# Optimization experiments

Hardware: AMD Instinct MI355X
Metric: run time of the kernel (lower is better)

The kernel has to match this reference:

```python
import jax, jax.numpy as jnp
import numpy as np

SEQ_LEN = 48
OUT_DIM = 3
EMB_DIM = 32
HID_DIM = 96
BATCH = 131072


def setup_inputs() -> dict:
    key = jax.random.key(0)
    ks = jax.random.split(key, 12)
    s_emb = 1.0 / np.sqrt(OUT_DIM)
    s_gru = 1.0 / np.sqrt(HID_DIM)
    s_out = 1.0 / np.sqrt(HID_DIM)
    u = lambda k, shp, s: jax.random.uniform(k, shp, jnp.float32, -s, s)
    return {
        "last_pos_rel": jax.random.normal(ks[0], (BATCH, OUT_DIM), jnp.float32),
        "past_encoded": jax.random.normal(ks[1], (1, BATCH, HID_DIM // 2), jnp.float32),
        "future_encoded": jax.random.normal(ks[2], (1, BATCH, HID_DIM // 2), jnp.float32),
        "W_emb": u(ks[3], (EMB_DIM, OUT_DIM), s_emb),
        "b_emb": u(ks[4], (EMB_DIM,), s_emb),
        "W_ih": u(ks[5], (3 * HID_DIM, EMB_DIM), s_gru),
        "W_hh": u(ks[6], (3 * HID_DIM, HID_DIM), s_gru),
        "b_ih": u(ks[7], (3 * HID_DIM,), s_gru),
        "b_hh": u(ks[8], (3 * HID_DIM,), s_gru),
        "W_out": u(ks[9], (OUT_DIM, HID_DIM), s_out),
        "b_out": u(ks[10], (OUT_DIM,), s_out),
    }


def reference(last_pos_rel, past_encoded, future_encoded, W_emb, b_emb,
              W_ih, W_hh, b_ih, b_hh, W_out, b_out):
    # initial hidden state: concat of the two 48-dim encodings -> (B, 96)
    h0 = jnp.concatenate([past_encoded, future_encoded], axis=2)[0]
    # initial decoder input: spatial embedding of last relative position
    x0 = last_pos_rel @ W_emb.T + b_emb  # (B, EMB)

    def step(carry, _):
        h, x = carry
        gx = x @ W_ih.T + b_ih   # (B, 3H)
        gh = h @ W_hh.T + b_hh   # (B, 3H)
        gxr, gxz, gxn = jnp.split(gx, 3, axis=-1)
        ghr, ghz, ghn = jnp.split(gh, 3, axis=-1)
        r = jax.nn.sigmoid(gxr + ghr)
        z = jax.nn.sigmoid(gxz + ghz)
        n = jnp.tanh(gxn + r * ghn)
        h_new = (1.0 - z) * n + z * h
        rel_pos = h_new @ W_out.T + b_out       # (B, 3)
        x_new = rel_pos @ W_emb.T + b_emb       # (B, EMB)
        return (h_new, x_new), rel_pos

    _, pred_traj = jax.lax.scan(step, (h0, x0), None, length=SEQ_LEN)
    return pred_traj  # (SEQ_LEN, B, 3)
```

## Files before the change

kernel.cpp:

```cpp
#include <hip/hip_runtime.h>
#include <hip/hip_bf16.h>
#include <type_traits>

#define SEQ_LEN 48
#define HID     96
#define NB      131072
#define MROWS   304
#define ABYTES  (MROWS*HID*2)
#define A_U4    (ABYTES/16)
#define COEF_OFF_F (ABYTES/4)
#define COEF_FLOATS (96*16)
#define BOUT_OFF_F (COEF_OFF_F + COEF_FLOATS)

typedef __attribute__((ext_vector_type(4))) float f32x4;
typedef __attribute__((ext_vector_type(8))) __bf16 bf16x8;
typedef unsigned int uint;
typedef unsigned short ushort;

__device__ __forceinline__ float sigm2(float xp) {
    return __builtin_amdgcn_rcpf(1.f + __builtin_amdgcn_exp2f(-xp));
}
__device__ __forceinline__ float tanh2(float yp) {
    return 1.f - 2.f * __builtin_amdgcn_rcpf(__builtin_amdgcn_exp2f(yp) + 1.f);
}
__device__ __forceinline__ uint packbf(float a, float b) {
    ushort lo = __builtin_bit_cast(ushort, __float2bfloat16(a));
    ushort hi = __builtin_bit_cast(ushort, __float2bfloat16(b));
    return (uint)lo | ((uint)hi << 16);
}

__global__ void fold_k(const float* __restrict__ W_emb, const float* __restrict__ b_emb,
                       const float* __restrict__ W_ih,  const float* __restrict__ W_hh,
                       const float* __restrict__ b_ih,  const float* __restrict__ b_hh,
                       const float* __restrict__ W_out, const float* __restrict__ b_out,
                       void* wsv)
{
    const float L2E  = 1.44269504088896340736f;
    const float L2E2 = 2.f * L2E;
    ushort* A  = (ushort*)wsv;
    float*  CF = (float*)wsv + COEF_OFF_F;
    float*  BO = (float*)wsv + BOUT_OFF_F;
    int g = blockIdx.x * 64 + threadIdx.x;
    if (g < 3) BO[g] = b_out[g];

    auto wxe_row = [&](int gg, float* w, float& bx) {
        w[0] = w[1] = w[2] = 0.f; bx = b_ih[gg];
        for (int e = 0; e < 32; e++) {
            float wi = W_ih[gg * 32 + e];
            w[0] += wi * W_emb[e * 3 + 0];
            w[1] += wi * W_emb[e * 3 + 1];
            w[2] += wi * W_emb[e * 3 + 2];
            bx   += wi * b_emb[e];
        }
    };

    if (g < MROWS) {
        float w[3] = {0.f, 0.f, 0.f}, bx = 0.f;
        if (g < 192) wxe_row(g, w, bx);
        for (int k = 0; k < HID; k++) {
            float val;
            if      (g < 192) val = (W_hh[g * HID + k] + w[0]*W_out[0*HID+k] + w[1]*W_out[1*HID+k] + w[2]*W_out[2*HID+k]) * L2E;
            else if (g < 288) val = W_hh[g * HID + k] * L2E2;
            else if (g < 291) val = W_out[(g - 288) * HID + k];
            else              val = 0.f;
            int t = g >> 4, c = k >> 5, l = (g & 15) | (((k >> 3) & 3) << 4), i = k & 7;
            A[((t * 3 + c) * 64 + l) * 8 + i] = __builtin_bit_cast(ushort, __float2bfloat16(val));
        }
    }
    if (g < 96) {
        int j = g;
        float wn[3], bxn; wxe_row(192 + j, wn, bxn);
        float wr[3], bxr; wxe_row(j,        wr, bxr);
        float wz[3], bxz; wxe_row(96 + j,   wz, bxz);
        float quads[4][4] = {
            { wn[0]*L2E2, wn[1]*L2E2, wn[2]*L2E2, bxn*L2E2 },
            { b_hh[192 + j]*L2E2,
              (bxr + b_hh[j]      + wr[0]*b_out[0] + wr[1]*b_out[1] + wr[2]*b_out[2]) * L2E,
              (bxz + b_hh[96 + j] + wz[0]*b_out[0] + wz[1]*b_out[1] + wz[2]*b_out[2]) * L2E,
              0.f },
            { wr[0]*L2E, wr[1]*L2E, wr[2]*L2E, wz[0]*L2E },
            { wz[1]*L2E, wz[2]*L2E, 0.f, 0.f }
        };
        int qj = (j >> 2) & 3;
        float* row = CF + j * 16;
        for (int L = 0; L < 4; ++L) {
            int p = (L + qj) & 3;
            row[p * 4 + 0] = quads[L][0];
            row[p * 4 + 1] = quads[L][1];
            row[p * 4 + 2] = quads[L][2];
            row[p * 4 + 3] = quads[L][3];
        }
    }
}

__global__ __launch_bounds__(256, 2)
void gru_mfma(const float* __restrict__ last_pos, const float* __restrict__ past,
              const float* __restrict__ fut, const void* __restrict__ wsv,
              float* __restrict__ out)
{
    __shared__ uint4 sb[A_U4];
    const int tid = threadIdx.x;
    const uint4* gsrc = (const uint4*)wsv;
    #pragma unroll
    for (int it = 0; it < 15; ++it) { int idx = tid + it * 256; if (idx < A_U4) sb[idx] = gsrc[idx]; }
    __syncthreads();

    const float* CF  = (const float*)wsv + COEF_OFF_F;
    const float* BOg = (const float*)wsv + BOUT_OFF_F;
    const float bo[3] = {BOg[0], BOg[1], BOg[2]};

    const int lane = tid & 63;
    const int wid  = tid >> 6;
    const int b    = lane & 15;
    const int q    = lane >> 4;
    const int rowbase = blockIdx.x * 128 + wid * 32;

    uint hpk[2][6][2];
    #pragma unroll
    for (int nt = 0; nt < 2; ++nt) {
        int row = rowbase + nt * 16 + b;
        #pragma unroll
        for (int t = 0; t < 6; ++t) {
            const float* src = (t < 3) ? (past + (size_t)row * 48 + t * 16 + q * 4)
                                       : (fut  + (size_t)row * 48 + (t - 3) * 16 + q * 4);
            f32x4 v = *(const f32x4*)src;
            hpk[nt][t][0] = packbf(v[0], v[1]);
            hpk[nt][t][1] = packbf(v[2], v[3]);
        }
    }

    const int idxA = 4 * (b | ((((q << 1) + 0) & 3) << 4));
    const int idxB = 4 * (b | ((((q << 1) + 1) & 3) << 4));
    uint4 bfu[2][3];
    auto do_exchange = [&]() {
        #pragma unroll
        for (int nt = 0; nt < 2; ++nt)
            #pragma unroll
            for (int c = 0; c < 3; ++c)
                #pragma unroll
                for (int dd = 0; dd < 4; ++dd) {
                    int idx = (dd < 2) ? idxA : idxB;
                    int va = __builtin_amdgcn_ds_bpermute(idx, (int)hpk[nt][2 * c][dd & 1]);
                    int vb = __builtin_amdgcn_ds_bpermute(idx, (int)hpk[nt][2 * c + 1][dd & 1]);
                    bfu[nt][c][dd] = (uint)((lane < 32) ? va : vb);
                }
    };
    do_exchange();

    float pc[2][3];
    #pragma unroll
    for (int nt = 0; nt < 2; ++nt) {
        int row = rowbase + nt * 16 + b;
        pc[nt][0] = last_pos[(size_t)row * 3 + 0];
        pc[nt][1] = last_pos[(size_t)row * 3 + 1];
        pc[nt][2] = last_pos[(size_t)row * 3 + 2];
    }

    const f32x4 zero4 = {0.f, 0.f, 0.f, 0.f};
    const int p0r = (0 + q) & 3, p1r = (1 + q) & 3, p2r = (2 + q) & 3, p3r = (3 + q) & 3;

    auto tile18 = [&](f32x4* a18) {
        #pragma unroll
        for (int c = 0; c < 3; ++c) {
            bf16x8 a = __builtin_bit_cast(bf16x8, sb[(18 * 3 + c) * 64 + lane]);
            #pragma unroll
            for (int nt = 0; nt < 2; ++nt) {
                bf16x8 bb = __builtin_bit_cast(bf16x8, bfu[nt][c]);
                a18[nt] = __builtin_amdgcn_mfma_f32_16x16x32_bf16(a, bb, (c == 0) ? zero4 : a18[nt], 0, 0, 0);
            }
        }
    };

    auto do_groups = [&](auto FIRST_c, const float (*d0)[3]) {
        constexpr bool FIRST = decltype(FIRST_c)::value;
        #pragma unroll
        for (int t = 0; t < 6; ++t) {
            f32x4 aR[2], aZ[2], aN[2];
            #pragma unroll
            for (int c = 0; c < 3; ++c) {
                bf16x8 fr = __builtin_bit_cast(bf16x8, sb[((t)      * 3 + c) * 64 + lane]);
                bf16x8 fz = __builtin_bit_cast(bf16x8, sb[((6 + t)  * 3 + c) * 64 + lane]);
                bf16x8 fn = __builtin_bit_cast(bf16x8, sb[((12 + t) * 3 + c) * 64 + lane]);
                #pragma unroll
                for (int nt = 0; nt < 2; ++nt) {
                    bf16x8 bb = __builtin_bit_cast(bf16x8, bfu[nt][c]);
                    aR[nt] = __builtin_amdgcn_mfma_f32_16x16x32_bf16(fr, bb, (c == 0) ? zero4 : aR[nt], 0, 0, 0);
                    aZ[nt] = __builtin_amdgcn_mfma_f32_16x16x32_bf16(fz, bb, (c == 0) ? zero4 : aZ[nt], 0, 0, 0);
                    aN[nt] = __builtin_amdgcn_mfma_f32_16x16x32_bf16(fn, bb, (c == 0) ? zero4 : aN[nt], 0, 0, 0);
                }
            }
            const float* cbase = CF + (16 * t + 4 * q) * 16;
            uint np[2][2] = {{0u, 0u}, {0u, 0u}};
            #pragma unroll
            for (int r = 0; r < 4; ++r) {
                f32x4 ca = *(const f32x4*)(cbase + 16 * r + 4 * p0r);
                f32x4 cb = *(const f32x4*)(cbase + 16 * r + 4 * p1r);
                #pragma unroll
                for (int nt = 0; nt < 2; ++nt) {
                    float sr  = aR[nt][r] + cb[1];
                    float sz  = aZ[nt][r] + cb[2];
                    float ghn = aN[nt][r] + cb[0];
                    float gxn = ca[3] + pc[nt][0]*ca[0] + pc[nt][1]*ca[1] + pc[nt][2]*ca[2];
                    if constexpr (FIRST) {
                        f32x4 c2 = *(const f32x4*)(cbase + 16 * r + 4 * p2r);
                        f32x4 c3 = *(const f32x4*)(cbase + 16 * r + 4 * p3r);
                        sr += d0[nt][0]*c2[0] + d0[nt][1]*c2[1] + d0[nt][2]*c2[2];
                        sz += d0[nt][0]*c2[3] + d0[nt][1]*c3[0] + d0[nt][2]*c3[1];
                    }
                    float rg = sigm2(sr);
                    float zg = sigm2(sz);
                    float ng = tanh2(gxn + rg * ghn);
                    uint pk = hpk[nt][t][r >> 1];
                    float hold = __builtin_bit_cast(float, (r & 1) ? (pk & 0xffff0000u) : (pk << 16));
                    float hv = ng + zg * (hold - ng);
                    ushort hb = __builtin_bit_cast(ushort, __float2bfloat16(hv));
                    np[nt][r >> 1] |= (uint)hb << (16 * (r & 1));
                }
            }
            #pragma unroll
            for (int nt = 0; nt < 2; ++nt) {
                hpk[nt][t][0] = np[nt][0];
                hpk[nt][t][1] = np[nt][1];
            }
            __builtin_amdgcn_sched_barrier(0);
        }
    };

    {
        f32x4 a18[2];
        tile18(a18);
        float d0[2][3];
        #pragma unroll
        for (int nt = 0; nt < 2; ++nt)
            #pragma unroll
            for (int o = 0; o < 3; ++o) {
                float po = a18[nt][o] + bo[o];
                float pb = __builtin_bit_cast(float,
                            __builtin_amdgcn_ds_bpermute(4 * b, __builtin_bit_cast(int, po)));
                d0[nt][o] = pc[nt][o] - pb;
            }
        __builtin_amdgcn_sched_barrier(0);
        do_groups(std::integral_constant<bool, true>{}, d0);
        do_exchange();
    }

    #pragma unroll 1
    for (int s = 1; s < SEQ_LEN; ++s) {
        f32x4 a18[2];
        tile18(a18);
        #pragma unroll
        for (int nt = 0; nt < 2; ++nt)
            #pragma unroll
            for (int o = 0; o < 3; ++o) {
                float po = a18[nt][o] + bo[o];
                float pb = __builtin_bit_cast(float,
                            __builtin_amdgcn_ds_bpermute(4 * b, __builtin_bit_cast(int, po)));
                if (q == 0) {
                    int row = rowbase + nt * 16 + b;
                    out[((size_t)(s - 1) * NB + row) * 3 + o] = po;
                }
                pc[nt][o] = pb;
            }
        __builtin_amdgcn_sched_barrier(0);
        do_groups(std::integral_constant<bool, false>{}, nullptr);
        do_exchange();
    }

    {
        f32x4 f18[2];
        tile18(f18);
        if (q == 0) {
            #pragma unroll
            for (int nt = 0; nt < 2; ++nt) {
                int row = rowbase + nt * 16 + b;
                #pragma unroll
                for (int o = 0; o < 3; ++o)
                    out[((size_t)47 * NB + row) * 3 + o] = f18[nt][o] + bo[o];
            }
        }
    }
}

extern "C" void kernel_launch(void* const* d_in, const int* in_sizes, int n_in,
                              void* d_out, int out_size, void* d_ws, size_t ws_size,
                              hipStream_t stream)
{
    const float* last_pos = (const float*)d_in[0];
    const float* past     = (const float*)d_in[1];
    const float* fut      = (const float*)d_in[2];
    const float* W_emb    = (const float*)d_in[3];
    const float* b_emb    = (const float*)d_in[4];
    const float* W_ih     = (const float*)d_in[5];
    const float* W_hh     = (const float*)d_in[6];
    const float* b_ih     = (const float*)d_in[7];
    const float* b_hh     = (const float*)d_in[8];
    const float* W_out    = (const float*)d_in[9];
    const float* b_out    = (const float*)d_in[10];
    float* out = (float*)d_out;

    hipLaunchKernelGGL(fold_k, dim3(5), dim3(64), 0, stream,
                       W_emb, b_emb, W_ih, W_hh, b_ih, b_hh, W_out, b_out, d_ws);
    hipLaunchKernelGGL(gru_mfma, dim3(NB / 128), dim3(256), 0, stream,
                       last_pos, past, fut, d_ws, out);
}
```

Before: 961.2 us.

## Fold input-gate n path into extra MFMA on hidden state, drop position broadcast

Folds the n-gate input contribution (W_ih_n·W_emb·W_out) into a new bf16 weight tile, so gxn is computed by an extra MFMA per group from the hidden state. This removes the per-step ds_bpermute broadcast of predicted positions and the scalar pc·coef FMAs. The first step keeps a correction through per-row PE coefficients. The cost is one more MFMA per tile, weight fragments read from global memory rather than LDS, and extra bf16 rounding on the gxn path.

```diff
diff --git a/kernel.cpp b/kernel.cpp
--- a/kernel.cpp
+++ b/kernel.cpp
@@ -8,9 +8,10 @@
 #define MROWS   304
 #define ABYTES  (MROWS*HID*2)
 #define A_U4    (ABYTES/16)
-#define COEF_OFF_F (ABYTES/4)
-#define COEF_FLOATS (96*16)
-#define BOUT_OFF_F (COEF_OFF_F + COEF_FLOATS)
+#define GX_OFF_U4 3648
+#define CB_OFF_F  19200
+#define PE_OFF_F  19584
+#define BO_OFF_F  20736
 
 typedef __attribute__((ext_vector_type(4))) float f32x4;
 typedef __attribute__((ext_vector_type(8))) __bf16 bf16x8;
@@ -37,9 +38,11 @@
 {
     const float L2E  = 1.44269504088896340736f;
     const float L2E2 = 2.f * L2E;
-    ushort* A  = (ushort*)wsv;
-    float*  CF = (float*)wsv + COEF_OFF_F;
-    float*  BO = (float*)wsv + BOUT_OFF_F;
+    ushort* A   = (ushort*)wsv;
+    ushort* GXu = (ushort*)wsv + ABYTES/2;
+    float*  CB  = (float*)wsv + CB_OFF_F;
+    float*  PE  = (float*)wsv + PE_OFF_F;
+    float*  BO  = (float*)wsv + BO_OFF_F;
     int g = blockIdx.x * 64 + threadIdx.x;
     if (g < 3) BO[g] = b_out[g];
 
@@ -72,24 +75,18 @@
         float wn[3], bxn; wxe_row(192 + j, wn, bxn);
         float wr[3], bxr; wxe_row(j,        wr, bxr);
         float wz[3], bxz; wxe_row(96 + j,   wz, bxz);
-        float quads[4][4] = {
-            { wn[0]*L2E2, wn[1]*L2E2, wn[2]*L2E2, bxn*L2E2 },
-            { b_hh[192 + j]*L2E2,
-              (bxr + b_hh[j]      + wr[0]*b_out[0] + wr[1]*b_out[1] + wr[2]*b_out[2]) * L2E,
-              (bxz + b_hh[96 + j] + wz[0]*b_out[0] + wz[1]*b_out[1] + wz[2]*b_out[2]) * L2E,
-              0.f },
-            { wr[0]*L2E, wr[1]*L2E, wr[2]*L2E, wz[0]*L2E },
-            { wz[1]*L2E, wz[2]*L2E, 0.f, 0.f }
-        };
-        int qj = (j >> 2) & 3;
-        float* row = CF + j * 16;
-        for (int L = 0; L < 4; ++L) {
-            int p = (L + qj) & 3;
-            row[p * 4 + 0] = quads[L][0];
-            row[p * 4 + 1] = quads[L][1];
-            row[p * 4 + 2] = quads[L][2];
-            row[p * 4 + 3] = quads[L][3];
-        }
+        for (int k = 0; k < HID; k++) {
+            float v = L2E2 * (wn[0]*W_out[0*HID+k] + wn[1]*W_out[1*HID+k] + wn[2]*W_out[2*HID+k]);
+            int t2 = j >> 4, c = k >> 5, l = (j & 15) | (((k >> 3) & 3) << 4), i = k & 7;
+            GXu[((t2 * 3 + c) * 64 + l) * 8 + i] = __builtin_bit_cast(ushort, __float2bfloat16(v));
+        }
+        CB[j*4 + 0] = b_hh[192 + j] * L2E2;
+        CB[j*4 + 1] = (bxr + b_hh[j]      + wr[0]*b_out[0] + wr[1]*b_out[1] + wr[2]*b_out[2]) * L2E;
+        CB[j*4 + 2] = (bxz + b_hh[96 + j] + wz[0]*b_out[0] + wz[1]*b_out[1] + wz[2]*b_out[2]) * L2E;
+        CB[j*4 + 3] = (bxn + wn[0]*b_out[0] + wn[1]*b_out[1] + wn[2]*b_out[2]) * L2E2;
+        PE[j*12 + 0] = wr[0]*L2E;  PE[j*12 + 1] = wr[1]*L2E;  PE[j*12 + 2] = wr[2]*L2E;  PE[j*12 + 3] = wz[0]*L2E;
+        PE[j*12 + 4] = wz[1]*L2E;  PE[j*12 + 5] = wz[2]*L2E;  PE[j*12 + 6] = wn[0]*L2E2; PE[j*12 + 7] = wn[1]*L2E2;
+        PE[j*12 + 8] = wn[2]*L2E2; PE[j*12 + 9] = 0.f;        PE[j*12 +10] = 0.f;        PE[j*12 +11] = 0.f;
     }
 }
 
@@ -105,8 +102,10 @@
     for (int it = 0; it < 15; ++it) { int idx = tid + it * 256; if (idx < A_U4) sb[idx] = gsrc[idx]; }
     __syncthreads();
 
-    const float* CF  = (const float*)wsv + COEF_OFF_F;
-    const float* BOg = (const float*)wsv + BOUT_OFF_F;
+    const uint4* GX  = (const uint4*)wsv + GX_OFF_U4;
+    const float* CBg = (const float*)wsv + CB_OFF_F;
+    const float* PEg = (const float*)wsv + PE_OFF_F;
+    const float* BOg = (const float*)wsv + BO_OFF_F;
     const float bo[3] = {BOg[0], BOg[1], BOg[2]};
 
     const int lane = tid & 63;
@@ -147,17 +146,7 @@
     };
     do_exchange();
 
-    float pc[2][3];
-    #pragma unroll
-    for (int nt = 0; nt < 2; ++nt) {
-        int row = rowbase + nt * 16 + b;
-        pc[nt][0] = last_pos[(size_t)row * 3 + 0];
-        pc[nt][1] = last_pos[(size_t)row * 3 + 1];
-        pc[nt][2] = last_pos[(size_t)row * 3 + 2];
-    }
-
     const f32x4 zero4 = {0.f, 0.f, 0.f, 0.f};
-    const int p0r = (0 + q) & 3, p1r = (1 + q) & 3, p2r = (2 + q) & 3, p3r = (3 + q) & 3;
 
     auto tile18 = [&](f32x4* a18) {
         #pragma unroll
@@ -175,37 +164,43 @@
         constexpr bool FIRST = decltype(FIRST_c)::value;
         #pragma unroll
         for (int t = 0; t < 6; ++t) {
-            f32x4 aR[2], aZ[2], aN[2];
+            f32x4 aR[2], aZ[2], aN[2], aX[2];
             #pragma unroll
             for (int c = 0; c < 3; ++c) {
                 bf16x8 fr = __builtin_bit_cast(bf16x8, sb[((t)      * 3 + c) * 64 + lane]);
                 bf16x8 fz = __builtin_bit_cast(bf16x8, sb[((6 + t)  * 3 + c) * 64 + lane]);
                 bf16x8 fn = __builtin_bit_cast(bf16x8, sb[((12 + t) * 3 + c) * 64 + lane]);
+                bf16x8 fx = __builtin_bit_cast(bf16x8, GX[(t * 3 + c) * 64 + lane]);
                 #pragma unroll
                 for (int nt = 0; nt < 2; ++nt) {
                     bf16x8 bb = __builtin_bit_cast(bf16x8, bfu[nt][c]);
                     aR[nt] = __builtin_amdgcn_mfma_f32_16x16x32_bf16(fr, bb, (c == 0) ? zero4 : aR[nt], 0, 0, 0);
                     aZ[nt] = __builtin_amdgcn_mfma_f32_16x16x32_bf16(fz, bb, (c == 0) ? zero4 : aZ[nt], 0, 0, 0);
                     aN[nt] = __builtin_amdgcn_mfma_f32_16x16x32_bf16(fn, bb, (c == 0) ? zero4 : aN[nt], 0, 0, 0);
+                    aX[nt] = __builtin_amdgcn_mfma_f32_16x16x32_bf16(fx, bb, (c == 0) ? zero4 : aX[nt], 0, 0, 0);
                 }
             }
-            const float* cbase = CF + (16 * t + 4 * q) * 16;
             uint np[2][2] = {{0u, 0u}, {0u, 0u}};
             #pragma unroll
             for (int r = 0; r < 4; ++r) {
-                f32x4 ca = *(const f32x4*)(cbase + 16 * r + 4 * p0r);
-                f32x4 cb = *(const f32x4*)(cbase + 16 * r + 4 * p1r);
+                int j = 16 * t + 4 * q + r;
+                f32x4 cbq = *(const f32x4*)(CBg + j * 4);
+                f32x4 pe0, pe1, pe2;
+                if constexpr (FIRST) {
+                    pe0 = *(const f32x4*)(PEg + j * 12);
+                    pe1 = *(const f32x4*)(PEg + j * 12 + 4);
+                    pe2 = *(const f32x4*)(PEg + j * 12 + 8);
+                }
                 #pragma unroll
                 for (int nt = 0; nt < 2; ++nt) {
-                    float sr  = aR[nt][r] + cb[1];
-                    float sz  = aZ[nt][r] + cb[2];
-                    float ghn = aN[nt][r] + cb[0];
-                    float gxn = ca[3] + pc[nt][0]*ca[0] + pc[nt][1]*ca[1] + pc[nt][2]*ca[2];
+                    float sr  = aR[nt][r] + cbq[1];
+                    float sz  = aZ[nt][r] + cbq[2];
+                    float ghn = aN[nt][r] + cbq[0];
+                    float gxn = aX[nt][r] + cbq[3];
                     if constexpr (FIRST) {
-                        f32x4 c2 = *(const f32x4*)(cbase + 16 * r + 4 * p2r);
-                        f32x4 c3 = *(const f32x4*)(cbase + 16 * r + 4 * p3r);
-                        sr += d0[nt][0]*c2[0] + d0[nt][1]*c2[1] + d0[nt][2]*c2[2];
-                        sz += d0[nt][0]*c2[3] + d0[nt][1]*c3[0] + d0[nt][2]*c3[1];
+                        sr  += d0[nt][0]*pe0[0] + d0[nt][1]*pe0[1] + d0[nt][2]*pe0[2];
+                        sz  += d0[nt][0]*pe0[3] + d0[nt][1]*pe1[0] + d0[nt][2]*pe1[1];
+                        gxn += d0[nt][0]*pe1[2] + d0[nt][1]*pe1[3] + d0[nt][2]*pe2[0];
                     }
                     float rg = sigm2(sr);
                     float zg = sigm2(sz);
@@ -227,6 +222,14 @@
     };
 
     {
+        float pc[2][3];
+        #pragma unroll
+        for (int nt = 0; nt < 2; ++nt) {
+            int row = rowbase + nt * 16 + b;
+            pc[nt][0] = last_pos[(size_t)row * 3 + 0];
+            pc[nt][1] = last_pos[(size_t)row * 3 + 1];
+            pc[nt][2] = last_pos[(size_t)row * 3 + 2];
+        }
         f32x4 a18[2];
         tile18(a18);
         float d0[2][3];
@@ -248,19 +251,15 @@
     for (int s = 1; s < SEQ_LEN; ++s) {
         f32x4 a18[2];
         tile18(a18);
-        #pragma unroll
-        for (int nt = 0; nt < 2; ++nt)
-            #pragma unroll
-            for (int o = 0; o < 3; ++o) {
-                float po = a18[nt][o] + bo[o];
-                float pb = __builtin_bit_cast(float,
-                            __builtin_amdgcn_ds_bpermute(4 * b, __builtin_bit_cast(int, po)));
-                if (q == 0) {
-                    int row = rowbase + nt * 16 + b;
-                    out[((size_t)(s - 1) * NB + row) * 3 + o] = po;
-                }
-                pc[nt][o] = pb;
-            }
+        if (q == 0) {
+            #pragma unroll
+            for (int nt = 0; nt < 2; ++nt) {
+                int row = rowbase + nt * 16 + b;
+                #pragma unroll
+                for (int o = 0; o < 3; ++o)
+                    out[((size_t)(s - 1) * NB + row) * 3 + o] = a18[nt][o] + bo[o];
+            }
+        }
         __builtin_amdgcn_sched_barrier(0);
         do_groups(std::integral_constant<bool, false>{}, nullptr);
         do_exchange();
```

Result: no change. 947.2 us (-1.4%).
